# Kernel optimization log

Hardware: AMD Instinct MI355X
Metric: run time of the kernel (lower is better)

The kernel has to match this reference:

```python
import jax, jax.numpy as jnp
import numpy as np

N_NODES = 100000
N_EDGES = 1600000
HID = 128
HEADS = 8
DK = HID // HEADS
N_LAYERS = 4
IN_DIM = 32
N_CLASSES = 16


def _ln(x, g, b, eps=1e-5):
    mu = x.mean(-1, keepdims=True)
    var = x.var(-1, keepdims=True)
    return (x - mu) / jnp.sqrt(var + eps) * g + b


def setup_inputs() -> dict:
    key = jax.random.key(0)
    ks = jax.random.split(key, 24)
    s = 0.05
    inp = {
        'feat': jax.random.randint(ks[0], (N_NODES,), 0, IN_DIM, dtype=jnp.int32),
        'edge_src': jax.random.randint(ks[1], (N_EDGES,), 0, N_NODES, dtype=jnp.int32),
        'edge_dst': jnp.sort(jax.random.randint(ks[2], (N_EDGES,), 0, N_NODES, dtype=jnp.int32)),
        'emb': jax.random.normal(ks[3], (IN_DIM, HID), jnp.float32) * s,
        'Wq': jax.random.normal(ks[4], (N_LAYERS, HID, HID), jnp.float32) * s,
        'Wk': jax.random.normal(ks[5], (N_LAYERS, HID, HID), jnp.float32) * s,
        'Wv': jax.random.normal(ks[6], (N_LAYERS, HID, HID), jnp.float32) * s,
        'Wo': jax.random.normal(ks[7], (N_LAYERS, HID, HID), jnp.float32) * s,
        'bo': jnp.zeros((N_LAYERS, HID), jnp.float32),
        'ln1_g': jnp.ones((N_LAYERS, HID), jnp.float32),
        'ln1_b': jnp.zeros((N_LAYERS, HID), jnp.float32),
        'W1': jax.random.normal(ks[8], (N_LAYERS, HID, 2 * HID), jnp.float32) * s,
        'b1': jnp.zeros((N_LAYERS, 2 * HID), jnp.float32),
        'W2': jax.random.normal(ks[9], (N_LAYERS, 2 * HID, HID), jnp.float32) * s,
        'b2': jnp.zeros((N_LAYERS, HID), jnp.float32),
        'ln2_g': jnp.ones((N_LAYERS, HID), jnp.float32),
        'ln2_b': jnp.zeros((N_LAYERS, HID), jnp.float32),
        'mW0': jax.random.normal(ks[10], (HID, HID // 2), jnp.float32) * s,
        'mb0': jnp.zeros((HID // 2,), jnp.float32),
        'mW1': jax.random.normal(ks[11], (HID // 2, HID // 4), jnp.float32) * s,
        'mb1': jnp.zeros((HID // 4,), jnp.float32),
        'mW2': jax.random.normal(ks[12], (HID // 4, N_CLASSES), jnp.float32) * s,
        'mb2': jnp.zeros((N_CLASSES,), jnp.float32),
    }
    return inp


def reference(feat, edge_src, edge_dst, emb, Wq, Wk, Wv, Wo, bo, ln1_g, ln1_b,
              W1, b1, W2, b2, ln2_g, ln2_b, mW0, mb0, mW1, mb1, mW2, mb2):
    N = feat.shape[0]
    h = emb[feat]  # [N, HID] embedding gather
    inv_sqrt_dk = jnp.float32(1.0 / np.sqrt(DK))
    for l in range(Wq.shape[0]):
        h_in1 = h
        q = (h @ Wq[l]).reshape(N, HEADS, DK)
        k = (h @ Wk[l]).reshape(N, HEADS, DK)
        v = (h @ Wv[l]).reshape(N, HEADS, DK)
        # per-edge scores: K[src] . Q[dst], scaled, clipped, exponentiated
        sc = jnp.einsum('ehd,ehd->eh', k[edge_src], q[edge_dst]) * inv_sqrt_dk
        sc = jnp.exp(jnp.clip(sc, -5.0, 5.0))  # [E, HEADS]
        wV = jax.ops.segment_sum(sc[:, :, None] * v[edge_src], edge_dst, num_segments=N)
        z = jax.ops.segment_sum(sc, edge_dst, num_segments=N)
        attn = (wV / (z[:, :, None] + 1e-6)).reshape(N, HID)
        h = h_in1 + (attn @ Wo[l] + bo[l])  # residual + O proj
        h = _ln(h, ln1_g[l], ln1_b[l])
        h_in2 = h
        f = jax.nn.relu(h @ W1[l] + b1[l]) @ W2[l] + b2[l]
        h = _ln(h_in2 + f, ln2_g[l], ln2_b[l])
    # MLPReadout: HID -> HID/2 -> HID/4 -> n_classes
    h = jax.nn.relu(h @ mW0 + mb0)
    h = jax.nn.relu(h @ mW1 + mb1)
    return h @ mW2 + mb2
```

## Files before the change

kernel.cpp:

```cpp
#include <hip/hip_runtime.h>
#include <hip/hip_fp16.h>

#define HID 128
#define N_LAYERS 4
#define IN_DIM 32
#define N_CLASSES 16

typedef _Float16 f16x8 __attribute__((ext_vector_type(8)));
typedef float f32x2 __attribute__((ext_vector_type(2)));
typedef __attribute__((ext_vector_type(4))) float f32x4;
typedef unsigned int uint_t;

#if defined(__has_builtin)
#if __has_builtin(__builtin_amdgcn_cvt_pk_f32_fp8)
#define HAVE_CVT_FP8 1
#endif
#if __has_builtin(__builtin_amdgcn_cvt_pk_fp8_f32)
#define HAVE_ENC_FP8 1
#endif
#endif

__device__ __forceinline__ unsigned short f2bf(float f) {
    unsigned int u = __float_as_uint(f);
    return (unsigned short)((u + 0x7FFFu + ((u >> 16) & 1u)) >> 16);
}
__device__ __forceinline__ float2 up16(uint_t u) {
    __half2 h = *(__half2*)&u;
    return __half22float2(h);
}

__device__ __forceinline__ unsigned char f2e4m3(float f) {
    unsigned int u = __float_as_uint(f);
    unsigned char s = (unsigned char)((u >> 24) & 0x80u);
    unsigned int a = u & 0x7FFFFFFFu;
    if (a >= 0x43E00000u) return s | 0x7Eu;
    int exp = (int)(a >> 23) - 127;
    if (exp < -6) {
        int m = (int)rintf(__uint_as_float(a) * 512.f);
        return s | (unsigned char)m;
    }
    unsigned int lsb = (a >> 20) & 1u;
    a += 0x7FFFFu + lsb;
    int e8 = ((int)(a >> 23) - 127) + 7;
    unsigned int m8 = (a >> 20) & 7u;
    return s | (unsigned char)((e8 << 3) | (int)m8);
}
__device__ __forceinline__ float e4m32f(unsigned int b) {
    unsigned int s = (b & 0x80u) << 24;
    unsigned int E = (b >> 3) & 15u, m = b & 7u;
    if (E == 0) {
        float v = (float)m * 0.001953125f;
        return __uint_as_float(__float_as_uint(v) | s);
    }
    return __uint_as_float(s | ((E + 120u) << 23) | (m << 20));
}
__device__ __forceinline__ unsigned char enc8(float v) {
#ifdef HAVE_ENC_FP8
    int r = __builtin_amdgcn_cvt_pk_fp8_f32(v, v, 0, false);
    return (unsigned char)(r & 0xFF);
#else
    return f2e4m3(v);
#endif
}
__device__ __forceinline__ void dec8v(uint_t u, f32x2* o) {
#ifdef HAVE_CVT_FP8
    o[0] = __builtin_amdgcn_cvt_pk_f32_fp8(u, false);
    o[1] = __builtin_amdgcn_cvt_pk_f32_fp8(u, true);
#else
    o[0] = (f32x2){e4m32f(u & 255u), e4m32f((u >> 8) & 255u)};
    o[1] = (f32x2){e4m32f((u >> 16) & 255u), e4m32f(u >> 24)};
#endif
}

__device__ __forceinline__ int frag_off(int row, int c) {
    return ((c >> 5) << 10) + (((c >> 3) & 3) << 8) + (row << 4) + ((c & 7) << 1);
}

__global__ void detect_kernel(const unsigned int* __restrict__ ln1g, int* __restrict__ flag) {
    if (threadIdx.x == 0 && blockIdx.x == 0)
        *flag = (ln1g[0] == 0x3F800000u) ? 0 : 1;
}

#define NSM 11
struct SArgs {
    const void* src[NSM];
    float*      dst[NSM];
    int         cnt[NSM];
};

__global__ void conv_kernel(SArgs args, const int* __restrict__ flag) {
    int p = blockIdx.y;
    int n = args.cnt[p];
    int base = (blockIdx.x * 256 + threadIdx.x) * 4;
    if (base >= n) return;
    float* dst = args.dst[p];
    if (*flag) {
        const unsigned short* s = (const unsigned short*)args.src[p];
        #pragma unroll
        for (int j = 0; j < 4; ++j)
            dst[base + j] = __uint_as_float(((unsigned int)s[base + j]) << 16);
    } else {
        const float* s = (const float*)args.src[p];
        *(float4*)&dst[base] = *(const float4*)&s[base];
    }
}

#define NW 27
struct WArgs {
    const void* src[NW];
    int         soff[NW];
    _Float16*   dst[NW];
    int         K[NW];
    int         M[NW];
    int         mode[NW];
};

__global__ void wconv_kernel(WArgs a, const int* __restrict__ flag) {
    int p = blockIdx.y;
    int K = a.K[p], M = a.M[p], mode = a.mode[p];
    int idx = blockIdx.x * 256 + threadIdx.x;
    if (idx >= K * M) return;
    int k = idx / M, m = idx % M;
    float v;
    if (*flag)
        v = __uint_as_float(((unsigned int)((const unsigned short*)a.src[p])[a.soff[p] + idx]) << 16);
    else
        v = ((const float*)a.src[p])[a.soff[p] + idx];
    size_t off;
    if (mode == 0) {
        off = (size_t)m * K + k;
    } else {
        int ht, k2;
        if (mode == 1) { ht = m >> 5; k2 = k; }
        else           { ht = ((k >> 7) << 2) + (m >> 5); k2 = k & 127; }
        int frag = (((k2 >> 5) * 2 + ((m >> 4) & 1)) << 6) + (((k2 >> 3) & 3) << 4) + (m & 15);
        off = (size_t)ht * 4096 + frag * 8 + (k & 7);
    }
    a.dst[p][off] = (_Float16)v;
}

__global__ void csr_kernel(const int* __restrict__ dst, int* __restrict__ row_start,
                           int N, int E) {
    int n = blockIdx.x * 256 + threadIdx.x;
    if (n > N) return;
    int lo = 0, hi = E;
    while (lo < hi) {
        int mid = (lo + hi) >> 1;
        if (dst[mid] < n) lo = mid + 1; else hi = mid;
    }
    row_start[n] = lo;
}

__global__ void embed_kernel(const int* __restrict__ feat, const float* __restrict__ emb,
                             _Float16* __restrict__ h, int N) {
    int idx = blockIdx.x * 256 + threadIdx.x;
    if (idx >= N * 16) return;
    int n  = idx >> 4;
    int c8 = idx & 15;
    int f = feat[n];
    const float* s = &emb[(size_t)f * HID + c8 * 8];
    float4 a = *(const float4*)s;
    float4 b = *(const float4*)(s + 4);
    f16x8 o;
    o[0] = (_Float16)a.x; o[1] = (_Float16)a.y; o[2] = (_Float16)a.z; o[3] = (_Float16)a.w;
    o[4] = (_Float16)b.x; o[5] = (_Float16)b.y; o[6] = (_Float16)b.z; o[7] = (_Float16)b.w;
    *(f16x8*)&h[(size_t)n * HID + c8 * 8] = o;
}

__launch_bounds__(256)
__global__ void mfma_gemm_qkv(const _Float16* __restrict__ Ain,
                              const _Float16* __restrict__ Bt,
                              _Float16* __restrict__ q16, unsigned char* __restrict__ kvp8) {
    __shared__ __align__(16) char As[16384];
    __shared__ __align__(16) char Bs[49152];

    const int t    = threadIdx.x;
    const int w    = t >> 6;
    const int l    = t & 63;
    const int quad = l >> 4;
    const int lc   = l & 15;
    const int row0 = blockIdx.x * 64;
    const int mbase = blockIdx.y * 192;

    char* Aw = As + (w << 12);

    #pragma unroll
    for (int i = 0; i < 4; ++i) {
        int idx = i * 64 + l;
        int row = idx >> 4, g = idx & 15;
        uint4 v = *(const uint4*)(Ain + (size_t)(row0 + w * 16 + row) * 128 + g * 8);
        *(uint4*)(Aw + ((g >> 2) << 10) + ((g & 3) << 8) + (row << 4)) = v;
    }
    {
        const uint4* Bsrc = (const uint4*)(Bt + (size_t)(mbase / 32) * 4096);
        #pragma unroll
        for (int i = 0; i < 12; ++i) {
            int idx = t + i * 256;
            *(uint4*)&Bs[idx * 16] = Bsrc[idx];
        }
    }
    __syncthreads();

    f32x4 acc[12];
    #pragma unroll
    for (int i = 0; i < 12; ++i) acc[i] = (f32x4){0.f, 0.f, 0.f, 0.f};

    #pragma unroll
    for (int kk = 0; kk < 4; ++kk) {
        f16x8 af = *(const f16x8*)(Aw + (kk << 10) + (quad << 8) + (lc << 4));
        #pragma unroll
        for (int i = 0; i < 12; ++i) {
            f16x8 bf = *(const f16x8*)(Bs + (i >> 1) * 8192 +
                                       ((kk * 2 + (i & 1)) << 10) + (quad << 8) + (lc << 4));
            acc[i] = __builtin_amdgcn_mfma_f32_16x16x32_f16(af, bf, acc[i], 0, 0, 0);
        }
    }

    #pragma unroll
    for (int r = 0; r < 4; ++r) {
        int row = row0 + w * 16 + quad * 4 + r;
        #pragma unroll
        for (int i = 0; i < 12; ++i) {
            float v = acc[i][r];
            int gc = mbase + i * 16 + lc;
            if (gc < 128)      q16[(size_t)row * 128 + gc] = (_Float16)v;
            else if (gc < 256) kvp8[(size_t)row * 256 + (gc - 128)] = enc8(v);
            else               kvp8[(size_t)row * 256 + 128 + (gc - 256)] = enc8(v);
        }
    }
}

template<int NEXTM, bool RMODE>
__launch_bounds__(256, 3)
__global__ void layer_fused(_Float16* __restrict__ h,
                            const _Float16* __restrict__ Wo, const _Float16* __restrict__ W1,
                            const _Float16* __restrict__ W2,
                            const _Float16* __restrict__ Wn, const float* __restrict__ bn,
                            const float* __restrict__ bo,  const float* __restrict__ l1g,
                            const float* __restrict__ l1b, const float* __restrict__ b1,
                            const float* __restrict__ b2,  const float* __restrict__ l2g,
                            const float* __restrict__ l2b,
                            _Float16* __restrict__ q16,
                            const uint_t* __restrict__ kvin, unsigned char* __restrict__ kvout,
                            const int* __restrict__ esrc, const int* __restrict__ rows,
                            int N) {
    constexpr int NHT = NEXTM / 32;
    __shared__ __align__(16) char bufA[16384];
    __shared__ __align__(16) char bufH[16384];
    __shared__ __align__(16) char bufB[16384];

    const int t = threadIdx.x, w = t >> 6, l = t & 63;
    const int quad = l >> 4, lc = l & 15;
    const int row0 = blockIdx.x * 64;
    char* Aw = bufA + (w << 12);
    char* Hw = bufH + (w << 12);

    auto ISSUE = [&](const _Float16* src, int bsel) {
        char* d = bufB + bsel * 8192 + w * 2048;
        const char* g = (const char*)src + w * 2048 + l * 16;
        __builtin_amdgcn_global_load_lds(
            (const __attribute__((address_space(1))) unsigned int*)g,
            (__attribute__((address_space(3))) unsigned int*)d, 16, 0, 0);
        __builtin_amdgcn_global_load_lds(
            (const __attribute__((address_space(1))) unsigned int*)(g + 1024),
            (__attribute__((address_space(3))) unsigned int*)(d + 1024), 16, 0, 0);
    };
    auto LDA = [&](const char* Ar, f16x8* afc) {
        #pragma unroll
        for (int kk = 0; kk < 4; ++kk)
            afc[kk] = *(const f16x8*)(Ar + (kk << 10) + (quad << 8) + (lc << 4));
    };
    auto MF2 = [&](const f16x8* afc, int bsel, f32x4* ac) {
        const char* B = bufB + bsel * 8192;
        #pragma unroll
        for (int kk = 0; kk < 4; ++kk) {
            #pragma unroll
            for (int i = 0; i < 2; ++i) {
                f16x8 bf = *(const f16x8*)(B + ((kk * 2 + i) << 10) + (quad << 8) + (lc << 4));
                ac[i] = __builtin_amdgcn_mfma_f32_16x16x32_f16(afc[kk], bf, ac[i], 0, 0, 0);
            }
        }
    };

    ISSUE(Wo, 0);

    _Float16 resv[4][8];
    #pragma unroll
    for (int r = 0; r < 4; ++r) {
        int row = row0 + w * 16 + quad * 4 + r;
        #pragma unroll
        for (int j = 0; j < 8; ++j)
            resv[r][j] = h[(size_t)row * 128 + j * 16 + lc];
    }

    {
        const int head = l & 7;
        const int rsub = l >> 3;
        #pragma unroll
        for (int task = 0; task < 2; ++task) {
            const int rr   = rsub + task * 8;
            const int node = row0 + w * 16 + rr;
            f16x8 o0, o1;
            #pragma unroll
            for (int j = 0; j < 8; ++j) { o0[j] = (_Float16)0; o1[j] = (_Float16)0; }
            if (node < N) {
                f32x2 qh[8];
                {
                    const uint4* qp = (const uint4*)(q16 + (size_t)node * HID + head * 16);
                    uint4 q0 = qp[0], q1 = qp[1];
                    uint_t qs[8] = {q0.x, q0.y, q0.z, q0.w, q1.x, q1.y, q1.z, q1.w};
                    #pragma unroll
                    for (int i = 0; i < 8; ++i) {
                        float2 f = up16(qs[i]);
                        qh[i] = (f32x2){f.x * 0.25f, f.y * 0.25f};
                    }
                }
                int e0 = rows[node], e1 = rows[node + 1];
                f32x2 wv[8];
                #pragma unroll
                for (int i = 0; i < 8; ++i) wv[i] = (f32x2){0.f, 0.f};
                float z = 0.f;

                uint4 ka = {0,0,0,0}, va = {0,0,0,0}, kc = {0,0,0,0}, vc = {0,0,0,0};
                bool oka = e0 < e1, okc = e0 + 1 < e1;
                if (oka) {
                    int sa = esrc[e0];
                    int sc = okc ? esrc[e0 + 1] : sa;
                    ka = *(const uint4*)(kvin + (size_t)sa * 64 + head * 4);
                    va = *(const uint4*)(kvin + (size_t)sa * 64 + 32 + head * 4);
                    kc = *(const uint4*)(kvin + (size_t)sc * 64 + head * 4);
                    vc = *(const uint4*)(kvin + (size_t)sc * 64 + 32 + head * 4);
                }
                for (int e = e0; e < e1; e += 2) {
                    uint4 cka = ka, cva = va, ckc = kc, cvc = vc;
                    bool coka = oka, cokc = okc;
                    int en = e + 2;
                    oka = en < e1; okc = en + 1 < e1;
                    if (oka) {
                        int sa = esrc[en];
                        int sc = okc ? esrc[en + 1] : sa;
                        ka = *(const uint4*)(kvin + (size_t)sa * 64 + head * 4);
                        va = *(const uint4*)(kvin + (size_t)sa * 64 + 32 + head * 4);
                        kc = *(const uint4*)(kvin + (size_t)sc * 64 + head * 4);
                        vc = *(const uint4*)(kvin + (size_t)sc * 64 + 32 + head * 4);
                    }
                    f32x2 k2a[8], k2c[8];
                    dec8v(cka.x, k2a); dec8v(cka.y, k2a + 2); dec8v(cka.z, k2a + 4); dec8v(cka.w, k2a + 6);
                    dec8v(ckc.x, k2c); dec8v(ckc.y, k2c + 2); dec8v(ckc.z, k2c + 4); dec8v(ckc.w, k2c + 6);
                    f32x2 da2 = (f32x2){0.f, 0.f}, dc2 = (f32x2){0.f, 0.f};
                    #pragma unroll
                    for (int j = 0; j < 8; ++j) { da2 += qh[j] * k2a[j]; dc2 += qh[j] * k2c[j]; }
                    float da = da2.x + da2.y, dc = dc2.x + dc2.y;
                    float sa2 = coka ? __expf(fminf(fmaxf(da, -5.f), 5.f)) : 0.f;
                    float sc2 = cokc ? __expf(fminf(fmaxf(dc, -5.f), 5.f)) : 0.f;

                    f32x2 v2a[8], v2c[8];
                    dec8v(cva.x, v2a); dec8v(cva.y, v2a + 2); dec8v(cva.z, v2a + 4); dec8v(cva.w, v2a + 6);
                    dec8v(cvc.x, v2c); dec8v(cvc.y, v2c + 2); dec8v(cvc.z, v2c + 4); dec8v(cvc.w, v2c + 6);
                    f32x2 pa = (f32x2){sa2, sa2}, pc = (f32x2){sc2, sc2};
                    #pragma unroll
                    for (int j = 0; j < 8; ++j) { wv[j] += pa * v2a[j]; wv[j] += pc * v2c[j]; }
                    z += sa2 + sc2;
                }
                float inv = 1.f / (z + 1e-6f);
                #pragma unroll
                for (int i = 0; i < 4; ++i) {
                    o0[2*i]   = (_Float16)(wv[i].x * inv);
                    o0[2*i+1] = (_Float16)(wv[i].y * inv);
                    o1[2*i]   = (_Float16)(wv[4+i].x * inv);
                    o1[2*i+1] = (_Float16)(wv[4+i].y * inv);
                }
            }
            *(f16x8*)(Aw + frag_off(rr, head * 16))     = o0;
            *(f16x8*)(Aw + frag_off(rr, head * 16 + 8)) = o1;
        }
    }

    f16x8 afA[4];
    LDA(Aw, afA);

    __syncthreads();
    int bb = 0;

    f32x4 acc[8];
    #pragma unroll
    for (int i = 0; i < 8; ++i) acc[i] = (f32x4){0.f, 0.f, 0.f, 0.f};
    #pragma unroll
    for (int c = 0; c < 4; ++c) {
        ISSUE(c < 3 ? Wo + (c + 1) * 4096 : W1, bb ^ 1);
        MF2(afA, bb, acc + c * 2);
        __syncthreads();
        bb ^= 1;
    }

    {
        float gv[8], bv[8], bb8[8];
        #pragma unroll
        for (int j = 0; j < 8; ++j) {
            int col = j * 16 + lc;
            gv[j] = l1g[col]; bv[j] = l1b[col]; bb8[j] = bo[col];
        }
        #pragma unroll
        for (int r = 0; r < 4; ++r) {
            float v[8];
            float s = 0.f, ss = 0.f;
            #pragma unroll
            for (int j = 0; j < 8; ++j) {
                v[j] = acc[j][r] + bb8[j] + (float)resv[r][j];
                s += v[j]; ss += v[j] * v[j];
            }
            #pragma unroll
            for (int m = 1; m <= 8; m <<= 1) { s += __shfl_xor(s, m); ss += __shfl_xor(ss, m); }
            float mu   = s * (1.f / 128.f);
            float rstd = rsqrtf(ss * (1.f / 128.f) - mu * mu + 1e-5f);
            #pragma unroll
            for (int j = 0; j < 8; ++j) {
                float o = (v[j] - mu) * rstd * gv[j] + bv[j];
                *(_Float16*)(Hw + frag_off(quad * 4 + r, j * 16 + lc)) = (_Float16)o;
            }
        }
    }

    f16x8 afH[4];
    LDA(Hw, afH);

    f32x4 acc3[8];
    #pragma unroll
    for (int i = 0; i < 8; ++i) acc3[i] = (f32x4){0.f, 0.f, 0.f, 0.f};
    #pragma unroll
    for (int hh = 0; hh < 2; ++hh) {
        #pragma unroll
        for (int j = 0; j < 4; ++j) {
            ISSUE(j < 3 ? W1 + (hh * 4 + j + 1) * 4096 : W2 + (hh * 4) * 4096, bb ^ 1);
            f32x4 a2[2];
            a2[0] = (f32x4){0.f, 0.f, 0.f, 0.f};
            a2[1] = (f32x4){0.f, 0.f, 0.f, 0.f};
            MF2(afH, bb, a2);
            #pragma unroll
            for (int r = 0; r < 4; ++r) {
                #pragma unroll
                for (int i2 = 0; i2 < 2; ++i2) {
                    float v = a2[i2][r] + b1[(hh * 4 + j) * 32 + i2 * 16 + lc];
                    v = fmaxf(v, 0.f);
                    *(_Float16*)(Aw + frag_off(quad * 4 + r, j * 32 + i2 * 16 + lc)) = (_Float16)v;
                }
            }
            __syncthreads();
            bb ^= 1;
        }
        f16x8 afT[4];
        LDA(Aw, afT);
        #pragma unroll
        for (int j = 0; j < 4; ++j) {
            const _Float16* nxt;
            if (j < 3)          nxt = W2 + (hh * 4 + j + 1) * 4096;
            else if (hh == 0)   nxt = W1 + 4 * 4096;
            else                nxt = Wn;
            ISSUE(nxt, bb ^ 1);
            MF2(afT, bb, acc3 + j * 2);
            __syncthreads();
            bb ^= 1;
        }
    }

    f16x8 ov[4];
    {
        float gv[8], bv[8], bb8[8];
        #pragma unroll
        for (int j = 0; j < 8; ++j) {
            int col = j * 16 + lc;
            gv[j] = l2g[col]; bv[j] = l2b[col]; bb8[j] = b2[col];
        }
        #pragma unroll
        for (int r = 0; r < 4; ++r) {
            float v[8];
            float s = 0.f, ss = 0.f;
            #pragma unroll
            for (int j = 0; j < 8; ++j) {
                float res = (float)*(const _Float16*)(Hw + frag_off(quad * 4 + r, j * 16 + lc));
                v[j] = acc3[j][r] + bb8[j] + res;
                s += v[j]; ss += v[j] * v[j];
            }
            #pragma unroll
            for (int m = 1; m <= 8; m <<= 1) { s += __shfl_xor(s, m); ss += __shfl_xor(ss, m); }
            float mu   = s * (1.f / 128.f);
            float rstd = rsqrtf(ss * (1.f / 128.f) - mu * mu + 1e-5f);
            #pragma unroll
            for (int j = 0; j < 8; ++j) {
                float o = (v[j] - mu) * rstd * gv[j] + bv[j];
                ov[r][j] = (_Float16)o;
                *(_Float16*)(Aw + frag_off(quad * 4 + r, j * 16 + lc)) = (_Float16)o;
            }
        }
    }

    LDA(Aw, afA);

    auto storeP = [&](int p, const f32x4* pf) {
        #pragma unroll
        for (int r = 0; r < 4; ++r) {
            int row = row0 + w * 16 + quad * 4 + r;
            #pragma unroll
            for (int i2 = 0; i2 < 2; ++i2) {
                int gc = p * 32 + i2 * 16 + lc;
                float v = pf[i2][r];
                if (RMODE) {
                    v += bn[gc];
                    v = fmaxf(v, 0.f);
                    q16[(size_t)row * 64 + gc] = (_Float16)v;
                } else {
                    if (gc < 128)      q16[(size_t)row * 128 + gc] = (_Float16)v;
                    else if (gc < 256) kvout[(size_t)row * 256 + (gc - 128)] = enc8(v);
                    else               kvout[(size_t)row * 256 + 128 + (gc - 256)] = enc8(v);
                }
            }
        }
    };

    f32x4 pf[2];
    #pragma unroll
    for (int c = 0; c < NHT; ++c) {
        if (c + 1 < NHT) ISSUE(Wn + (c + 1) * 4096, bb ^ 1);
        if (c == 0) {
            #pragma unroll
            for (int r = 0; r < 4; ++r) {
                int row = row0 + w * 16 + quad * 4 + r;
                #pragma unroll
                for (int j = 0; j < 8; ++j)
                    h[(size_t)row * 128 + j * 16 + lc] = ov[r][j];
            }
        } else {
            storeP(c - 1, pf);
        }
        f32x4 a4[2];
        a4[0] = (f32x4){0.f, 0.f, 0.f, 0.f};
        a4[1] = (f32x4){0.f, 0.f, 0.f, 0.f};
        MF2(afA, bb, a4);
        if (c + 1 < NHT) __syncthreads();
        bb ^= 1;
        pf[0] = a4[0]; pf[1] = a4[1];
    }
    storeP(NHT - 1, pf);
}

__launch_bounds__(256)
__global__ void readout_tail(const _Float16* __restrict__ r0,
                             const _Float16* __restrict__ w1t, const float* __restrict__ b1_,
                             const _Float16* __restrict__ w2t, const float* __restrict__ b2_,
                             void* __restrict__ outp, const int* __restrict__ flag, int N) {
    constexpr int SA = 144;
    constexpr int SR = 80;
    __shared__ __align__(16) char bufA[64 * SA];
    __shared__ __align__(16) char bufR[64 * SR];

    const int t    = threadIdx.x;
    const int w    = t >> 6;
    const int l    = t & 63;
    const int quad = l >> 4;
    const int lc   = l & 15;
    const int row0 = blockIdx.x * 64;

    #pragma unroll
    for (int i = 0; i < 2; ++i) {
        int idx = t + i * 256;
        int r = idx >> 3, u = idx & 7;
        *(uint4*)&bufA[r * SA + u * 16] = *(const uint4*)(r0 + (size_t)(row0 + r) * 64 + u * 8);
    }
    __syncthreads();

    f32x4 acc[2];
    acc[0] = (f32x4){0.f, 0.f, 0.f, 0.f};
    acc[1] = (f32x4){0.f, 0.f, 0.f, 0.f};
    #pragma unroll
    for (int kk = 0; kk < 2; ++kk) {
        f16x8 af = *(const f16x8*)&bufA[(w * 16 + lc) * SA + kk * 64 + quad * 16];
        #pragma unroll
        for (int i = 0; i < 2; ++i) {
            f16x8 bf = *(const f16x8*)(w1t + (size_t)(i * 16 + lc) * 64 + kk * 32 + quad * 8);
            acc[i] = __builtin_amdgcn_mfma_f32_16x16x32_f16(af, bf, acc[i], 0, 0, 0);
        }
    }
    #pragma unroll
    for (int r = 0; r < 4; ++r) {
        int lrow = (w * 16 + quad * 4 + r) * SR;
        #pragma unroll
        for (int i = 0; i < 2; ++i) {
            float v = acc[i][r] + b1_[i * 16 + lc];
            v = fmaxf(v, 0.f);
            *(_Float16*)&bufR[lrow + (i * 16 + lc) * 2] = (_Float16)v;
        }
    }
    __syncthreads();
    f32x4 a2 = (f32x4){0.f, 0.f, 0.f, 0.f};
    {
        f16x8 af = *(const f16x8*)&bufR[(w * 16 + lc) * SR + quad * 16];
        f16x8 bf = *(const f16x8*)(w2t + (size_t)lc * 32 + quad * 8);
        a2 = __builtin_amdgcn_mfma_f32_16x16x32_f16(af, bf, a2, 0, 0, 0);
    }
    #pragma unroll
    for (int r = 0; r < 4; ++r) {
        int row = row0 + w * 16 + quad * 4 + r;
        if (row < N) {
            float v = a2[r] + b2_[lc];
            size_t o = (size_t)row * 16 + lc;
            if (*flag) ((unsigned short*)outp)[o] = f2bf(v);
            else       ((float*)outp)[o] = v;
        }
    }
}

extern "C" void kernel_launch(void* const* d_in, const int* in_sizes, int n_in,
                              void* d_out, int out_size, void* d_ws, size_t ws_size,
                              hipStream_t stream) {
    const int N  = in_sizes[0];
    const int E  = in_sizes[1];
    const int RB = (N + 63) / 64;
    const size_t NP = (size_t)RB * 64;

    const int* d_feat = (const int*)d_in[0];
    const int* d_esrc = (const int*)d_in[1];
    const int* d_edst = (const int*)d_in[2];

    char* base = (char*)d_ws;
    size_t cur = 0;
    auto alloc = [&](size_t bytes) -> char* {
        cur = (cur + 255) & ~(size_t)255;
        char* p = base + cur;
        cur += bytes;
        return p;
    };
    int* d_flag = (int*)alloc(4);
    int* d_rows = (int*)alloc((size_t)(N + 1) * 4);

    float* p_emb = (float*)alloc(IN_DIM * HID * 4);
    float* p_bo  = (float*)alloc(N_LAYERS * HID * 4);
    float* p_l1g = (float*)alloc(N_LAYERS * HID * 4);
    float* p_l1b = (float*)alloc(N_LAYERS * HID * 4);
    float* p_b1  = (float*)alloc(N_LAYERS * 2 * HID * 4);
    float* p_b2  = (float*)alloc(N_LAYERS * HID * 4);
    float* p_l2g = (float*)alloc(N_LAYERS * HID * 4);
    float* p_l2b = (float*)alloc(N_LAYERS * HID * 4);
    float* p_mb0 = (float*)alloc(64 * 4);
    float* p_mb1 = (float*)alloc(32 * 4);
    float* p_mb2 = (float*)alloc(16 * 4);

    _Float16* wqkv_t = (_Float16*)alloc((size_t)N_LAYERS * 384 * 128 * 2);
    _Float16* wo_t   = (_Float16*)alloc((size_t)N_LAYERS * 128 * 128 * 2);
    _Float16* w1_t   = (_Float16*)alloc((size_t)N_LAYERS * 256 * 128 * 2);
    _Float16* w2_t   = (_Float16*)alloc((size_t)N_LAYERS * 128 * 256 * 2);
    _Float16* mw0_t  = (_Float16*)alloc(64 * 128 * 2);
    _Float16* mw1_t  = (_Float16*)alloc(32 * 64 * 2);
    _Float16* mw2_t  = (_Float16*)alloc(16 * 32 * 2);

    _Float16*      buf_h = (_Float16*)alloc(NP * HID * 2);
    _Float16*      q16   = (_Float16*)alloc(NP * HID * 2);
    unsigned char* kv0   = (unsigned char*)alloc(NP * 256);
    unsigned char* kv1   = (unsigned char*)alloc(NP * 256);

    detect_kernel<<<1, 64, 0, stream>>>((const unsigned int*)d_in[9], d_flag);

    {
        SArgs sa;
        const int sidx[NSM] = {3, 8, 9, 10, 12, 14, 15, 16, 18, 20, 22};
        float*    sdst[NSM] = {p_emb, p_bo, p_l1g, p_l1b, p_b1, p_b2, p_l2g, p_l2b, p_mb0, p_mb1, p_mb2};
        const int scnt[NSM] = {IN_DIM*HID, N_LAYERS*HID, N_LAYERS*HID, N_LAYERS*HID,
                               N_LAYERS*2*HID, N_LAYERS*HID, N_LAYERS*HID, N_LAYERS*HID, 64, 32, 16};
        for (int i = 0; i < NSM; ++i) { sa.src[i] = d_in[sidx[i]]; sa.dst[i] = sdst[i]; sa.cnt[i] = scnt[i]; }
        conv_kernel<<<dim3(4, NSM), 256, 0, stream>>>(sa, d_flag);
    }

    {
        WArgs wa;
        int wi = 0;
        auto addw = [&](int inp, int off, int Kd, int Md, _Float16* dst, int mode) {
            wa.src[wi] = d_in[inp]; wa.soff[wi] = off; wa.K[wi] = Kd; wa.M[wi] = Md;
            wa.dst[wi] = dst; wa.mode[wi] = mode; ++wi;
        };
        for (int l = 0; l < N_LAYERS; ++l) {
            addw(4,  l * 16384, 128, 128, wqkv_t + (size_t)l * 49152, 1);
            addw(5,  l * 16384, 128, 128, wqkv_t + (size_t)l * 49152 + 16384, 1);
            addw(6,  l * 16384, 128, 128, wqkv_t + (size_t)l * 49152 + 32768, 1);
            addw(7,  l * 16384, 128, 128, wo_t + (size_t)l * 16384, 1);
            addw(11, l * 32768, 128, 256, w1_t + (size_t)l * 32768, 1);
            addw(13, l * 32768, 256, 128, w2_t + (size_t)l * 32768, 2);
        }
        addw(17, 0, 128, 64, mw0_t, 1);
        addw(19, 0, 64,  32, mw1_t, 0);
        addw(21, 0, 32,  16, mw2_t, 0);
        wconv_kernel<<<dim3(128, NW), 256, 0, stream>>>(wa, d_flag);
    }

    csr_kernel<<<(N + 1 + 255) / 256, 256, 0, stream>>>(d_edst, d_rows, N, E);
    embed_kernel<<<((size_t)N * 16 + 255) / 256, 256, 0, stream>>>(d_feat, p_emb, buf_h, N);

    mfma_gemm_qkv<<<dim3(RB, 2), 256, 0, stream>>>(buf_h, wqkv_t, q16, kv0);

    for (int l = 0; l < N_LAYERS; ++l) {
        const _Float16* Wo = wo_t + (size_t)l * 16384;
        const _Float16* W1 = w1_t + (size_t)l * 32768;
        const _Float16* W2 = w2_t + (size_t)l * 32768;
        const float* bo  = p_bo  + (size_t)l * HID;
        const float* l1g = p_l1g + (size_t)l * HID;
        const float* l1b = p_l1b + (size_t)l * HID;
        const float* b1  = p_b1  + (size_t)l * 2 * HID;
        const float* b2  = p_b2  + (size_t)l * HID;
        const float* l2g = p_l2g + (size_t)l * HID;
        const float* l2b = p_l2b + (size_t)l * HID;

        const uint_t*  kvin  = (const uint_t*)((l & 1) ? kv1 : kv0);
        unsigned char* kvout = (l & 1) ? kv0 : kv1;

        if (l < N_LAYERS - 1) {
            layer_fused<384, false><<<RB, 256, 0, stream>>>(
                buf_h, Wo, W1, W2, wqkv_t + (size_t)(l + 1) * 49152, nullptr,
                bo, l1g, l1b, b1, b2, l2g, l2b, q16, kvin, kvout, d_esrc, d_rows, N);
        } else {
            layer_fused<64, true><<<RB, 256, 0, stream>>>(
                buf_h, Wo, W1, W2, mw0_t, p_mb0,
                bo, l1g, l1b, b1, b2, l2g, l2b, q16, kvin, kvout, d_esrc, d_rows, N);
        }
    }

    readout_tail<<<RB, 256, 0, stream>>>(q16, mw1_t, p_mb1, mw2_t, p_mb2, d_out, d_flag, N);
}
```

Measured before the change: 731.2 us.

## Load weight fragments directly into registers, dropping LDS staging and barriers

Weight tiles for the fused layer GEMMs are now read straight from global memory into per-thread register fragments, double-buffered in registers, instead of being staged in shared memory with async global-to-LDS loads. This removes the shared weight buffer and every block-wide barrier in the GEMM chain. The aim is less LDS traffic and synchronisation, plus possibly higher occupancy. In exchange, each wave loads the same weights redundantly from global/L2, and the two 8-vector register buffers raise register pressure under the 3-blocks-per-SM launch bound.

```diff
diff --git a/kernel.cpp b/kernel.cpp
--- a/kernel.cpp
+++ b/kernel.cpp
@@ -247,7 +247,6 @@
     constexpr int NHT = NEXTM / 32;
     __shared__ __align__(16) char bufA[16384];
     __shared__ __align__(16) char bufH[16384];
-    __shared__ __align__(16) char bufB[16384];
 
     const int t = threadIdx.x, w = t >> 6, l = t & 63;
     const int quad = l >> 4, lc = l & 15;
@@ -255,34 +254,24 @@
     char* Aw = bufA + (w << 12);
     char* Hw = bufH + (w << 12);
 
-    auto ISSUE = [&](const _Float16* src, int bsel) {
-        char* d = bufB + bsel * 8192 + w * 2048;
-        const char* g = (const char*)src + w * 2048 + l * 16;
-        __builtin_amdgcn_global_load_lds(
-            (const __attribute__((address_space(1))) unsigned int*)g,
-            (__attribute__((address_space(3))) unsigned int*)d, 16, 0, 0);
-        __builtin_amdgcn_global_load_lds(
-            (const __attribute__((address_space(1))) unsigned int*)(g + 1024),
-            (__attribute__((address_space(3))) unsigned int*)(d + 1024), 16, 0, 0);
-    };
     auto LDA = [&](const char* Ar, f16x8* afc) {
         #pragma unroll
         for (int kk = 0; kk < 4; ++kk)
             afc[kk] = *(const f16x8*)(Ar + (kk << 10) + (quad << 8) + (lc << 4));
     };
-    auto MF2 = [&](const f16x8* afc, int bsel, f32x4* ac) {
-        const char* B = bufB + bsel * 8192;
+    auto LDB = [&](f16x8* rb, const _Float16* B) {
+        #pragma unroll
+        for (int f = 0; f < 8; ++f)
+            rb[f] = *(const f16x8*)((const char*)B + (f << 10) + (quad << 8) + (lc << 4));
+    };
+    auto MF2R = [&](const f16x8* afc, const f16x8* rb, f32x4* ac) {
         #pragma unroll
         for (int kk = 0; kk < 4; ++kk) {
             #pragma unroll
-            for (int i = 0; i < 2; ++i) {
-                f16x8 bf = *(const f16x8*)(B + ((kk * 2 + i) << 10) + (quad << 8) + (lc << 4));
-                ac[i] = __builtin_amdgcn_mfma_f32_16x16x32_f16(afc[kk], bf, ac[i], 0, 0, 0);
-            }
+            for (int i = 0; i < 2; ++i)
+                ac[i] = __builtin_amdgcn_mfma_f32_16x16x32_f16(afc[kk], rb[kk * 2 + i], ac[i], 0, 0, 0);
         }
     };
-
-    ISSUE(Wo, 0);
 
     _Float16 resv[4][8];
     #pragma unroll
@@ -379,18 +368,17 @@
     f16x8 afA[4];
     LDA(Aw, afA);
 
-    __syncthreads();
-    int bb = 0;
+    f16x8 rb0[8], rb1[8];
+    LDB(rb0, Wo);
 
     f32x4 acc[8];
     #pragma unroll
     for (int i = 0; i < 8; ++i) acc[i] = (f32x4){0.f, 0.f, 0.f, 0.f};
     #pragma unroll
     for (int c = 0; c < 4; ++c) {
-        ISSUE(c < 3 ? Wo + (c + 1) * 4096 : W1, bb ^ 1);
-        MF2(afA, bb, acc + c * 2);
-        __syncthreads();
-        bb ^= 1;
+        const _Float16* nxt = (c < 3) ? Wo + (c + 1) * 4096 : W1;
+        if ((c & 1) == 0) { LDB(rb1, nxt); MF2R(afA, rb0, acc + c * 2); }
+        else              { LDB(rb0, nxt); MF2R(afA, rb1, acc + c * 2); }
     }
 
     {
@@ -421,21 +409,21 @@
         }
     }
 
-    f16x8 afH[4];
-    LDA(Hw, afH);
-
     f32x4 acc3[8];
     #pragma unroll
     for (int i = 0; i < 8; ++i) acc3[i] = (f32x4){0.f, 0.f, 0.f, 0.f};
     #pragma unroll
     for (int hh = 0; hh < 2; ++hh) {
+        f16x8 afH[4];
+        LDA(Hw, afH);
         #pragma unroll
         for (int j = 0; j < 4; ++j) {
-            ISSUE(j < 3 ? W1 + (hh * 4 + j + 1) * 4096 : W2 + (hh * 4) * 4096, bb ^ 1);
+            const _Float16* nxt = (j < 3) ? W1 + (hh * 4 + j + 1) * 4096 : W2 + (hh * 4) * 4096;
             f32x4 a2[2];
             a2[0] = (f32x4){0.f, 0.f, 0.f, 0.f};
             a2[1] = (f32x4){0.f, 0.f, 0.f, 0.f};
-            MF2(afH, bb, a2);
+            if ((j & 1) == 0) { LDB(rb1, nxt); MF2R(afH, rb0, a2); }
+            else              { LDB(rb0, nxt); MF2R(afH, rb1, a2); }
             #pragma unroll
             for (int r = 0; r < 4; ++r) {
                 #pragma unroll
@@ -445,8 +433,6 @@
                     *(_Float16*)(Aw + frag_off(quad * 4 + r, j * 32 + i2 * 16 + lc)) = (_Float16)v;
                 }
             }
-            __syncthreads();
-            bb ^= 1;
         }
         f16x8 afT[4];
         LDA(Aw, afT);
@@ -456,10 +442,8 @@
             if (j < 3)          nxt = W2 + (hh * 4 + j + 1) * 4096;
             else if (hh == 0)   nxt = W1 + 4 * 4096;
             else                nxt = Wn;
-            ISSUE(nxt, bb ^ 1);
-            MF2(afT, bb, acc3 + j * 2);
-            __syncthreads();
-            bb ^= 1;
+            if ((j & 1) == 0) { LDB(rb1, nxt); MF2R(afT, rb0, acc3 + j * 2); }
+            else              { LDB(rb0, nxt); MF2R(afT, rb1, acc3 + j * 2); }
         }
     }
 
@@ -520,7 +504,16 @@
     f32x4 pf[2];
     #pragma unroll
     for (int c = 0; c < NHT; ++c) {
-        if (c + 1 < NHT) ISSUE(Wn + (c + 1) * 4096, bb ^ 1);
+        f32x4 a4[2];
+        a4[0] = (f32x4){0.f, 0.f, 0.f, 0.f};
+        a4[1] = (f32x4){0.f, 0.f, 0.f, 0.f};
+        if ((c & 1) == 0) {
+            if (c + 1 < NHT) LDB(rb1, Wn + (c + 1) * 4096);
+            MF2R(afA, rb0, a4);
+        } else {
+            if (c + 1 < NHT) LDB(rb0, Wn + (c + 1) * 4096);
+            MF2R(afA, rb1, a4);
+        }
         if (c == 0) {
             #pragma unroll
             for (int r = 0; r < 4; ++r) {
@@ -532,12 +525,6 @@
         } else {
             storeP(c - 1, pf);
         }
-        f32x4 a4[2];
-        a4[0] = (f32x4){0.f, 0.f, 0.f, 0.f};
-        a4[1] = (f32x4){0.f, 0.f, 0.f, 0.f};
-        MF2(afA, bb, a4);
-        if (c + 1 < NHT) __syncthreads();
-        bb ^= 1;
         pf[0] = a4[0]; pf[1] = a4[1];
     }
     storeP(NHT - 1, pf);
```

Result: slower. 748.6 us (+2.4%).
